# Kernel tuning notes

Measured on AMD Instinct MI355X. Metric: run time of the kernel, lower is better.

## Reference

```python
import jax, jax.numpy as jnp
import numpy as np

B, T, E, H = 4, 2048, 1024, 16
HS = E // H  # head_size = 64
FFN_HID = 100  # hard-coded in FeedForward
EPS = 1e-5


def layernorm(x, g, b):
    mu = jnp.mean(x, axis=-1, keepdims=True)
    var = jnp.mean(jnp.square(x - mu), axis=-1, keepdims=True)
    return (x - mu) * jax.lax.rsqrt(var + EPS) * g + b


def setup_inputs() -> dict:
    key = jax.random.key(0)
    ks = jax.random.split(key, 10)
    s = E ** -0.5
    return {
        "x": jax.random.normal(ks[0], (B, T, E), jnp.float32),
        "wq": jax.random.normal(ks[1], (E, E), jnp.float32) * s,
        "wk": jax.random.normal(ks[2], (E, E), jnp.float32) * s,
        "wv": jax.random.normal(ks[3], (E, E), jnp.float32) * s,
        "w_proj": jax.random.normal(ks[4], (E, E), jnp.float32) * s,
        "b_proj": jnp.zeros((E,), jnp.float32),
        "w1": jax.random.normal(ks[5], (E, FFN_HID), jnp.float32) * s,
        "b1": jnp.zeros((FFN_HID,), jnp.float32),
        "w2": jax.random.normal(ks[6], (FFN_HID, E), jnp.float32) * (FFN_HID ** -0.5),
        "b2": jnp.zeros((E,), jnp.float32),
        "ln1_g": jnp.ones((E,), jnp.float32),
        "ln1_b": jnp.zeros((E,), jnp.float32),
        "ln2_g": jnp.ones((E,), jnp.float32),
        "ln2_b": jnp.zeros((E,), jnp.float32),
    }


def reference(x, wq, wk, wv, w_proj, b_proj, w1, b1, w2, b2, ln1_g, ln1_b, ln2_g, ln2_b):
    # --- self-attention with pre-LN residual ---
    h = layernorm(x, ln1_g, ln1_b)  # [B,T,E]
    def split_heads(y):  # [B,T,E] -> [B,H,T,HS]
        return y.reshape(B, T, H, HS).transpose(0, 2, 1, 3)
    q = split_heads(h @ wq)
    k = split_heads(h @ wk)
    v = split_heads(h @ wv)
    # NOTE: original scales by C**-0.5 with C = n_embd (not head_size)
    wei = jnp.einsum("bhtd,bhsd->bhts", q, k) * (E ** -0.5)  # [B,H,T,T]
    causal = jnp.tril(jnp.ones((T, T), bool))
    wei = jnp.where(causal, wei, -jnp.inf)
    wei = jax.nn.softmax(wei, axis=-1)
    att = jnp.einsum("bhts,bhsd->bhtd", wei, v)  # [B,H,T,HS]
    att = att.transpose(0, 2, 1, 3).reshape(B, T, E)  # concat heads
    x = x + att @ w_proj + b_proj
    # --- feedforward with pre-LN residual ---
    h2 = layernorm(x, ln2_g, ln2_b)
    ff = jax.nn.relu(h2 @ w1 + b1) @ w2 + b2
    return x + ff
```

## Files before the change

### kernel.cpp

```cpp
#include <hip/hip_runtime.h>

typedef unsigned short u16;
typedef unsigned int u32;
typedef __bf16 bf16x8 __attribute__((ext_vector_type(8)));
typedef float f32x4 __attribute__((ext_vector_type(4)));

#define BDIM 4
#define TDIM 2048
#define EDIM 1024
#define HDIM 16
#define HS 64
#define MROWS (BDIM * TDIM)
#define FFNP 128

__device__ __forceinline__ u16 f2bf(float f) {
    __bf16 h = (__bf16)f;
    return __builtin_bit_cast(u16, h);
}

__device__ __forceinline__ float bf2f(u16 u) {
    return (float)__builtin_bit_cast(__bf16, u);
}

__device__ __forceinline__ void glds16(const void* g, void* l) {
    __builtin_amdgcn_global_load_lds(
        (__attribute__((address_space(1))) const void*)g,
        (__attribute__((address_space(3))) void*)l, 16, 0, 0);
}

__global__ __launch_bounds__(256) void transpose_all(
    const float* __restrict__ wq, const float* __restrict__ wk,
    const float* __restrict__ wv, const float* __restrict__ wproj,
    const float* __restrict__ w1, const float* __restrict__ w2,
    u16* __restrict__ wqkvt, u16* __restrict__ wpt,
    u16* __restrict__ w1t, u16* __restrict__ w2t)
{
    __shared__ u16 sm[64][72];
    const float* src; u16* dst;
    int K, N, Kpad, Npad;
    switch (blockIdx.z) {
        case 0: src = wq;    dst = wqkvt;                 K = N = Kpad = Npad = 1024; break;
        case 1: src = wk;    dst = wqkvt + 1024 * 1024;   K = N = Kpad = Npad = 1024; break;
        case 2: src = wv;    dst = wqkvt + 2 * 1024 * 1024; K = N = Kpad = Npad = 1024; break;
        case 3: src = wproj; dst = wpt;                   K = N = Kpad = Npad = 1024; break;
        case 4: src = w1;    dst = w1t; K = 1024; N = 100; Kpad = 1024; Npad = 128; break;
        default: src = w2;   dst = w2t; K = 100; N = 1024; Kpad = 128; Npad = 1024; break;
    }
    int k0 = blockIdx.x * 64, n0 = blockIdx.y * 64;
    if (k0 >= Kpad || n0 >= Npad) return;
    int tid = threadIdx.x;
#pragma unroll
    for (int i = 0; i < 16; i++) {
        int idx = i * 256 + tid;
        int kl = idx >> 6, nl = idx & 63;
        int k = k0 + kl, n = n0 + nl;
        float v = (k < K && n < N) ? src[(size_t)k * N + n] : 0.f;
        sm[kl][nl] = f2bf(v);
    }
    __syncthreads();
#pragma unroll
    for (int i = 0; i < 16; i++) {
        int idx = i * 256 + tid;
        int nl = idx >> 6, kl = idx & 63;
        int n = n0 + nl, k = k0 + kl;
        if (n < Npad && k < Kpad) dst[(size_t)n * Kpad + k] = sm[kl][nl];
    }
}

__global__ __launch_bounds__(256) void ln_rows(
    const float* __restrict__ X, const float* __restrict__ G,
    const float* __restrict__ Bv, u16* __restrict__ H)
{
    int w = threadIdx.x >> 6, l = threadIdx.x & 63;
    int row = blockIdx.x * 4 + w;
    const float* xr = X + (size_t)row * EDIM;
    float4 v[4];
    float s = 0.f, s2 = 0.f;
#pragma unroll
    for (int i = 0; i < 4; i++) {
        v[i] = *(const float4*)&xr[l * 4 + i * 256];
        s += v[i].x + v[i].y + v[i].z + v[i].w;
        s2 += v[i].x * v[i].x + v[i].y * v[i].y + v[i].z * v[i].z + v[i].w * v[i].w;
    }
#pragma unroll
    for (int off = 1; off < 64; off <<= 1) {
        s += __shfl_xor(s, off, 64);
        s2 += __shfl_xor(s2, off, 64);
    }
    float mean = s * (1.f / EDIM);
    float var = s2 * (1.f / EDIM) - mean * mean;
    float rstd = rsqrtf(var + 1e-5f);
#pragma unroll
    for (int i = 0; i < 4; i++) {
        int c = l * 4 + i * 256;
        float4 gg = *(const float4*)&G[c];
        float4 bb = *(const float4*)&Bv[c];
        u16 o0 = f2bf((v[i].x - mean) * rstd * gg.x + bb.x);
        u16 o1 = f2bf((v[i].y - mean) * rstd * gg.y + bb.y);
        u16 o2 = f2bf((v[i].z - mean) * rstd * gg.z + bb.z);
        u16 o3 = f2bf((v[i].w - mean) * rstd * gg.w + bb.w);
        uint2 pk;
        pk.x = (u32)o0 | ((u32)o1 << 16);
        pk.y = (u32)o2 | ((u32)o3 << 16);
        *(uint2*)&H[(size_t)row * EDIM + c] = pk;
    }
}

__global__ __launch_bounds__(256) void ln_rows_b(
    const u16* __restrict__ X, const float* __restrict__ G,
    const float* __restrict__ Bv, u16* __restrict__ H)
{
    int w = threadIdx.x >> 6, l = threadIdx.x & 63;
    int row = blockIdx.x * 4 + w;
    const u16* xr = X + (size_t)row * EDIM;
    float v[16];
    float s = 0.f, s2 = 0.f;
#pragma unroll
    for (int i = 0; i < 2; i++) {
        bf16x8 u = *(const bf16x8*)&xr[l * 8 + i * 512];
#pragma unroll
        for (int e = 0; e < 8; e++) {
            float f = (float)u[e];
            v[i * 8 + e] = f;
            s += f; s2 += f * f;
        }
    }
#pragma unroll
    for (int off = 1; off < 64; off <<= 1) {
        s += __shfl_xor(s, off, 64);
        s2 += __shfl_xor(s2, off, 64);
    }
    float mean = s * (1.f / EDIM);
    float var = s2 * (1.f / EDIM) - mean * mean;
    float rstd = rsqrtf(var + 1e-5f);
#pragma unroll
    for (int i = 0; i < 2; i++) {
        int c = l * 8 + i * 512;
        float4 g0 = *(const float4*)&G[c];
        float4 g1 = *(const float4*)&G[c + 4];
        float4 b0 = *(const float4*)&Bv[c];
        float4 b1 = *(const float4*)&Bv[c + 4];
        float gg[8] = {g0.x, g0.y, g0.z, g0.w, g1.x, g1.y, g1.z, g1.w};
        float bb[8] = {b0.x, b0.y, b0.z, b0.w, b1.x, b1.y, b1.z, b1.w};
        uint4 pk;
        u32 o[8];
#pragma unroll
        for (int e = 0; e < 8; e++)
            o[e] = (u32)f2bf((v[i * 8 + e] - mean) * rstd * gg[e] + bb[e]);
        pk.x = o[0] | (o[1] << 16);
        pk.y = o[2] | (o[3] << 16);
        pk.z = o[4] | (o[5] << 16);
        pk.w = o[6] | (o[7] << 16);
        *(uint4*)&H[(size_t)row * EDIM + c] = pk;
    }
}

#define LDA4(d, mfb)                                                          \
    _Pragma("unroll") for (int mi = 0; mi < 4; mi++)                          \
    _Pragma("unroll") for (int ks = 0; ks < 2; ks++)                          \
        a[mi][ks] = *(const bf16x8*)&L[d][0][wm][((mfb + mi) * 16 + lr) * 64  \
                        + (((lg + 4 * ks) ^ (lr & 7)) << 3)];
#define LDB2(d, nfb)                                                          \
    _Pragma("unroll") for (int ni = 0; ni < 2; ni++)                          \
    _Pragma("unroll") for (int ks = 0; ks < 2; ks++)                          \
        b[ni][ks] = *(const bf16x8*)&L[d][1][wh][((wn & 1) * 64               \
                        + (nfb + ni) * 16 + lr) * 64                          \
                        + (((lg + 4 * ks) ^ (lr & 7)) << 3)];
#define MFMAQ(mfb, nfb)                                                       \
    _Pragma("unroll") for (int mi = 0; mi < 4; mi++)                          \
    _Pragma("unroll") for (int ni = 0; ni < 2; ni++)                          \
    _Pragma("unroll") for (int ks = 0; ks < 2; ks++)                          \
        acc[mfb + mi][nfb + ni] = __builtin_amdgcn_mfma_f32_16x16x32_bf16(    \
            a[mi][ks], b[ni][ks], acc[mfb + mi][nfb + ni], 0, 0, 0);
#define PH_SYNC1()                                                            \
    __builtin_amdgcn_s_barrier();                                             \
    asm volatile("s_waitcnt lgkmcnt(0)" ::: "memory");                        \
    __builtin_amdgcn_sched_barrier(0);                                        \
    __builtin_amdgcn_s_setprio(1);
#define PH_SYNC2()                                                            \
    __builtin_amdgcn_s_setprio(0);                                            \
    __builtin_amdgcn_s_barrier();
#define PH_SYNC2V(cond)                                                       \
    __builtin_amdgcn_s_setprio(0);                                            \
    if (cond) { asm volatile("s_waitcnt vmcnt(2)" ::: "memory"); }            \
    else      { asm volatile("s_waitcnt vmcnt(0)" ::: "memory"); }            \
    __builtin_amdgcn_s_barrier();

__global__ __launch_bounds__(512, 2) void gemm256_qk(
    const u16* __restrict__ A, const u16* __restrict__ Bt,
    u16* __restrict__ Cb)
{
    __shared__ u16 L[2][2][2][128 * 64];
    int id = blockIdx.x;
    int sw = (id & 7) * 32 + (id >> 3);
    int bx = sw % 32, by = sw / 32;
    const int m0 = bx * 256, n0 = by * 256;

    const int tid = threadIdx.x;
    const int w = tid >> 6, l = tid & 63;
    const int wm = w >> 2, wn = w & 3, wh = wn >> 1;
    const int lg = l >> 4, lr = l & 15;

    const int srow = w * 16 + (l >> 3);
    const int sch8 = ((l & 7) ^ (l >> 3)) * 8;

    auto stA = [&](int d, int h, int t) {
        const u16* src = A + (size_t)(m0 + h * 128 + srow) * 1024 + t * 64 + sch8;
        u16* dst = &L[d][0][h][w * 1024];
        glds16(src, dst);
        glds16(src + (size_t)8 * 1024, dst + 512);
    };
    auto stB = [&](int d, int h, int t) {
        const u16* src = Bt + (size_t)(n0 + h * 128 + srow) * 1024 + t * 64 + sch8;
        u16* dst = &L[d][1][h][w * 1024];
        glds16(src, dst);
        glds16(src + (size_t)8 * 1024, dst + 512);
    };

    f32x4 acc[8][4];
#pragma unroll
    for (int i = 0; i < 8; i++)
#pragma unroll
        for (int j = 0; j < 4; j++) acc[i][j] = f32x4{0.f, 0.f, 0.f, 0.f};
    bf16x8 a[4][2], b[2][2];

    const int NI = 1024 >> 7;

    stA(0, 0, 0); stA(0, 1, 0); stB(0, 0, 0); stB(0, 1, 0);
    stB(1, 0, 1);
    asm volatile("s_waitcnt vmcnt(2)" ::: "memory");
    __builtin_amdgcn_s_barrier();

#pragma unroll 1
    for (int j = 0; j < NI; j++) {
        const int t = 2 * j;
        const bool more = (j + 1 < NI);
        LDA4(0, 0); LDB2(0, 0);
        stA(1, 0, t + 1);
        PH_SYNC1(); MFMAQ(0, 0); PH_SYNC2();
        LDA4(0, 4);
        stA(1, 1, t + 1);
        PH_SYNC1(); MFMAQ(4, 0); PH_SYNC2();
        LDB2(0, 2);
        stB(1, 1, t + 1);
        PH_SYNC1(); MFMAQ(4, 2); PH_SYNC2();
        LDA4(0, 0);
        if (more) stB(0, 1, t + 2);
        PH_SYNC1(); MFMAQ(0, 2); PH_SYNC2V(more);
        LDA4(1, 0); LDB2(1, 0);
        if (more) stA(0, 0, t + 2);
        PH_SYNC1(); MFMAQ(0, 0); PH_SYNC2();
        LDA4(1, 4);
        if (more) stA(0, 1, t + 2);
        PH_SYNC1(); MFMAQ(4, 0); PH_SYNC2();
        LDB2(1, 2);
        if (more) stB(0, 0, t + 2);
        PH_SYNC1(); MFMAQ(4, 2); PH_SYNC2();
        LDA4(1, 0);
        if (more) stB(1, 0, t + 3);
        PH_SYNC1(); MFMAQ(0, 2); PH_SYNC2V(more);
    }

#pragma unroll
    for (int mf = 0; mf < 8; mf++) {
#pragma unroll
        for (int nf = 0; nf < 4; nf++) {
#pragma unroll
            for (int e = 0; e < 4; e++) {
                int row = m0 + wm * 128 + mf * 16 + lg * 4 + e;
                int col = n0 + wn * 64 + nf * 16 + lr;
                Cb[(size_t)row * 2048 + col] = f2bf(acc[mf][nf][e]);
            }
        }
    }
}

template <int MODE>
__global__ __launch_bounds__(256, 2) void gemm_bt(
    const u16* __restrict__ A, const u16* __restrict__ Bt,
    float* __restrict__ Cf,
    const void* __restrict__ resid, const float* __restrict__ bias,
    int M, int N, int K, int lda, int ldb, int mb)
{
    __shared__ u16 As[2][128 * 32];
    __shared__ u16 Bs[2][128 * 32];
    int bx, by;
    if constexpr (MODE == 4) {
        bx = blockIdx.x; by = blockIdx.y;
        int kz = blockIdx.z;
        A += kz * 256;
        Bt += kz * 256;
        Cf += (size_t)kz * M * N;
    } else {
        int nwg = gridDim.x, id = blockIdx.x;
        int sw = (id & 7) * (nwg >> 3) + (id >> 3);
        bx = sw % mb; by = sw / mb;
    }
    const int tid = threadIdx.x;
    const int w = tid >> 6, l = tid & 63;
    const int wr = w >> 1, wc = w & 1;
    const int lg = l >> 4, lr = l & 15;
    const int m0 = bx * 128, n0 = by * 128;

    f32x4 zero = {0.f, 0.f, 0.f, 0.f};
    f32x4 acc[4][4];
#pragma unroll
    for (int i = 0; i < 4; i++)
#pragma unroll
        for (int j = 0; j < 4; j++) acc[i][j] = zero;

    const u16* Ag = A + (size_t)(m0 + w * 16 + (l >> 2)) * lda + (l & 3) * 8;
    const u16* Bg = Bt + (size_t)(n0 + w * 16 + (l >> 2)) * ldb + (l & 3) * 8;

    auto stage = [&](int b, int k0) {
        glds16(Ag + k0, &As[b][w * 512]);
        glds16(Ag + k0 + (size_t)64 * lda, &As[b][w * 512 + 2048]);
        glds16(Bg + k0, &Bs[b][w * 512]);
        glds16(Bg + k0 + (size_t)64 * ldb, &Bs[b][w * 512 + 2048]);
    };
    auto compute = [&](int b) {
        bf16x8 af[4], bfr[4];
#pragma unroll
        for (int t = 0; t < 4; t++)
            af[t] = *(const bf16x8*)&As[b][(wr * 64 + t * 16 + lr) * 32 + lg * 8];
#pragma unroll
        for (int t = 0; t < 4; t++)
            bfr[t] = *(const bf16x8*)&Bs[b][(wc * 64 + t * 16 + lr) * 32 + lg * 8];
#pragma unroll
        for (int i = 0; i < 4; i++)
#pragma unroll
            for (int j = 0; j < 4; j++)
                acc[i][j] = __builtin_amdgcn_mfma_f32_16x16x32_bf16(
                    af[i], bfr[j], acc[i][j], 0, 0, 0);
    };

    stage(0, 0);
    __syncthreads();
    int cur = 0;
    for (int k0 = 32; k0 < K; k0 += 32) {
        stage(cur ^ 1, k0);
        compute(cur);
        __syncthreads();
        cur ^= 1;
    }
    compute(cur);

#pragma unroll
    for (int i = 0; i < 4; i++) {
#pragma unroll
        for (int j = 0; j < 4; j++) {
#pragma unroll
            for (int e = 0; e < 4; e++) {
                int row = m0 + wr * 64 + i * 16 + lg * 4 + e;
                int col = n0 + wc * 64 + j * 16 + lr;
                float v = acc[i][j][e];
                if constexpr (MODE == 2) {
                    size_t idx = (size_t)row * N + col;
                    ((u16*)Cf)[idx] =
                        f2bf(((const float*)resid)[idx] + v + bias[col]);
                } else if constexpr (MODE == 3) {
                    size_t idx = (size_t)row * N + col;
                    Cf[idx] = bf2f(((const u16*)resid)[idx]) + v + bias[col];
                } else if constexpr (MODE == 4) {
                    Cf[(size_t)row * N + col] = v;
                } else {
                    u16* vtp = (u16*)Cf;
                    int bq = col >> 11, tt = col & 2047;
                    vtp[((size_t)bq * 1024 + row) * 2048 + tt] = f2bf(v);
                }
            }
        }
    }
}

__global__ __launch_bounds__(256) void relu_reduce4(
    const float* __restrict__ fp, const float* __restrict__ b1,
    u16* __restrict__ tb)
{
    const size_t CH = (size_t)MROWS * FFNP;
    size_t base = ((size_t)blockIdx.x * 256 + threadIdx.x) * 4;
    float4 s0 = *(const float4*)&fp[base];
    float4 s1 = *(const float4*)&fp[base + CH];
    float4 s2 = *(const float4*)&fp[base + 2 * CH];
    float4 s3 = *(const float4*)&fp[base + 3 * CH];
    int col = (int)(base & (FFNP - 1));
    float sv[4] = {s0.x + s1.x + s2.x + s3.x, s0.y + s1.y + s2.y + s3.y,
                   s0.z + s1.z + s2.z + s3.z, s0.w + s1.w + s2.w + s3.w};
    u16 o[4];
#pragma unroll
    for (int j = 0; j < 4; j++) {
        int c = col + j;
        float b = (c < 100) ? b1[c] : 0.f;
        o[j] = f2bf(fmaxf(sv[j] + b, 0.f));
    }
    uint2 pk;
    pk.x = (u32)o[0] | ((u32)o[1] << 16);
    pk.y = (u32)o[2] | ((u32)o[3] << 16);
    *(uint2*)&tb[base] = pk;
}

__global__ __launch_bounds__(256, 4) void attn_fwd(
    const u16* __restrict__ qk, const u16* __restrict__ Vt,
    u16* __restrict__ Og)
{
    int xcd = blockIdx.x & 7;
    int j = blockIdx.x >> 3;
    int bh = xcd * 8 + (j & 7);
    int qp = j >> 3;
    int bb = bh >> 4, hh = bh & 15;

    int tid = threadIdx.x;
    int w = tid >> 6, l = tid & 63;
    int lg = l >> 4, lr = l & 15;

    const u16* Qb = qk + ((size_t)bb * TDIM) * 2048 + hh * HS;
    const u16* Kb = Qb + 1024;
    const u16* Vb = Vt + (size_t)bh * HS * TDIM;

    __shared__ u16 Ks[2][64 * 64];
    __shared__ u16 Vs[2][64 * 64];
    __shared__ __align__(16) u16 Ps[4][16 * 64];

    int srow = w * 16 + (l >> 3);
    int schunk = (l & 7) ^ ((l >> 3) & 7);
    u16* Pw = Ps[w];
    int sbase = (l & 48) + lg * 4;

    const float QSCL = 0.045084227f;

#pragma unroll 1
    for (int qi = 0; qi < 2; qi++) {
        int qb = (qi == 0 ? qp : 31 - qp) * 64;
        int q_abs = qb + w * 16 + lr;
        int wlo = qb + w * 16;
        int nt = qb / 64 + 1;

        bf16x8 qf[2];
        qf[0] = *(const bf16x8*)&Qb[(size_t)q_abs * 2048 + lg * 8];
        qf[1] = *(const bf16x8*)&Qb[(size_t)q_abs * 2048 + 32 + lg * 8];
#pragma unroll
        for (int i = 0; i < 8; i++) {
            qf[0][i] = (__bf16)((float)qf[0][i] * QSCL);
            qf[1][i] = (__bf16)((float)qf[1][i] * QSCL);
        }

        f32x4 zero = {0.f, 0.f, 0.f, 0.f};
        f32x4 oacc[4];
#pragma unroll
        for (int dt = 0; dt < 4; dt++) oacc[dt] = zero;
        float lpart = 0.f;

        auto stage = [&](int b, int kv0) {
            glds16(Kb + (size_t)(kv0 + srow) * 2048 + schunk * 8, &Ks[b][w * 1024]);
            glds16(Kb + (size_t)(kv0 + srow + 8) * 2048 + schunk * 8,
                   &Ks[b][w * 1024 + 512]);
            glds16(Vb + (size_t)srow * TDIM + kv0 + schunk * 8, &Vs[b][w * 1024]);
            glds16(Vb + (size_t)(srow + 8) * TDIM + kv0 + schunk * 8,
                   &Vs[b][w * 1024 + 512]);
        };

        stage(0, 0);
        if (nt > 1) stage(1, 64);
#pragma unroll 1
        for (int t = 0; t < nt; t++) {
            int kv0 = t * 64;
            int buf = t & 1;
            if (t + 1 < nt) { asm volatile("s_waitcnt vmcnt(4)" ::: "memory"); }
            else            { asm volatile("s_waitcnt vmcnt(0)" ::: "memory"); }
            __builtin_amdgcn_sched_barrier(0);
            __builtin_amdgcn_s_barrier();
            const u16* Kc = Ks[buf];
            const u16* Vc = Vs[buf];
            f32x4 sc[4];
#pragma unroll
            for (int ct = 0; ct < 4; ct++) sc[ct] = zero;
            __builtin_amdgcn_s_setprio(1);
#pragma unroll
            for (int ct = 0; ct < 4; ct++) {
#pragma unroll
                for (int dc = 0; dc < 2; dc++) {
                    bf16x8 kf = *(const bf16x8*)&Kc[(ct * 16 + lr) * 64 +
                                                    (((lg + 4 * dc) ^ (lr & 7)) << 3)];
                    sc[ct] = __builtin_amdgcn_mfma_f32_16x16x32_bf16(
                        kf, qf[dc], sc[ct], 0, 0, 0);
                }
            }
            __builtin_amdgcn_s_setprio(0);
            bf16x8 vfr[2][4];
#pragma unroll
            for (int m = 0; m < 2; m++)
#pragma unroll
                for (int dt = 0; dt < 4; dt++)
                    vfr[m][dt] = *(const bf16x8*)&Vc[(dt * 16 + lr) * 64 +
                                                     (((lg + 4 * m) ^ (lr & 7)) << 3)];
            float p[16];
            if (kv0 + 63 > wlo) {
#pragma unroll
                for (int ct = 0; ct < 4; ct++) {
#pragma unroll
                    for (int e = 0; e < 4; e++) {
                        float v = sc[ct][e];
                        if (kv0 + ct * 16 + lg * 4 + e > q_abs) v = -1e30f;
                        p[ct * 4 + e] = v;
                    }
                }
            } else {
#pragma unroll
                for (int ct = 0; ct < 4; ct++) {
#pragma unroll
                    for (int e = 0; e < 4; e++) p[ct * 4 + e] = sc[ct][e];
                }
            }
            float psum = 0.f;
#pragma unroll
            for (int i = 0; i < 16; i++) {
                p[i] = __builtin_amdgcn_exp2f(p[i]);
                psum += p[i];
            }
            lpart += psum;
#pragma unroll
            for (int ct = 0; ct < 4; ct++) {
                uint2 pr;
                pr.x = (u32)f2bf(p[ct * 4 + 0]) | ((u32)f2bf(p[ct * 4 + 1]) << 16);
                pr.y = (u32)f2bf(p[ct * 4 + 2]) | ((u32)f2bf(p[ct * 4 + 3]) << 16);
                int kvb = ct * 16 + lg * 4;
                int idx = lr * 64 + ((((kvb >> 3) ^ (lr & 7)) << 3) | (kvb & 7));
                *(uint2*)&Pw[idx] = pr;
            }
            asm volatile("s_waitcnt lgkmcnt(0)" ::: "memory");
            __builtin_amdgcn_sched_barrier(0);
            __builtin_amdgcn_s_setprio(1);
#pragma unroll
            for (int m = 0; m < 2; m++) {
                bf16x8 pa = *(const bf16x8*)&Pw[lr * 64 + (((lg + 4 * m) ^ (lr & 7)) << 3)];
#pragma unroll
                for (int dt = 0; dt < 4; dt++) {
                    oacc[dt] = __builtin_amdgcn_mfma_f32_16x16x32_bf16(
                        pa, vfr[m][dt], oacc[dt], 0, 0, 0);
                }
            }
            __builtin_amdgcn_s_setprio(0);
            __builtin_amdgcn_s_barrier();
            if (t + 2 < nt) stage(buf, kv0 + 128);
        }
        float lsum = lpart;
        lsum += __shfl_xor(lsum, 16, 64);
        lsum += __shfl_xor(lsum, 32, 64);
        float lT[4];
#pragma unroll
        for (int e = 0; e < 4; e++) lT[e] = __shfl(lsum, sbase + e, 64);
#pragma unroll
        for (int dt = 0; dt < 4; dt++) {
#pragma unroll
            for (int e = 0; e < 4; e++) {
                int row = qb + w * 16 + lg * 4 + e;
                Og[((size_t)bb * TDIM + row) * EDIM + hh * HS + dt * 16 + lr] =
                    f2bf(oacc[dt][e] / lT[e]);
            }
        }
    }
}

extern "C" void kernel_launch(void* const* d_in, const int* in_sizes, int n_in,
                              void* d_out, int out_size, void* d_ws, size_t ws_size,
                              hipStream_t stream)
{
    const float* x     = (const float*)d_in[0];
    const float* wq    = (const float*)d_in[1];
    const float* wk    = (const float*)d_in[2];
    const float* wv    = (const float*)d_in[3];
    const float* wproj = (const float*)d_in[4];
    const float* bproj = (const float*)d_in[5];
    const float* w1    = (const float*)d_in[6];
    const float* b1    = (const float*)d_in[7];
    const float* w2    = (const float*)d_in[8];
    const float* b2    = (const float*)d_in[9];
    const float* ln1g  = (const float*)d_in[10];
    const float* ln1b  = (const float*)d_in[11];
    const float* ln2g  = (const float*)d_in[12];
    const float* ln2b  = (const float*)d_in[13];
    float* out = (float*)d_out;

    char* ws = (char*)d_ws;
    size_t off = 0;
    auto alloc = [&](size_t bytes) -> void* {
        void* p = (void*)(ws + off);
        off += (bytes + 255) & ~(size_t)255;
        return p;
    };
    u16* hbuf = (u16*)alloc((size_t)MROWS * EDIM * 2);
    u16* qk   = (u16*)alloc((size_t)MROWS * 2048 * 2);
    u16* attb = (u16*)alloc((size_t)MROWS * EDIM * 2);
    u16* vt   = (u16*)alloc((size_t)MROWS * EDIM * 2);
    u16* x2b  = (u16*)alloc((size_t)MROWS * EDIM * 2);
    u16* wqkvt = (u16*)alloc((size_t)3072 * EDIM * 2);
    u16* wpt  = (u16*)alloc((size_t)EDIM * EDIM * 2);
    u16* w1t  = (u16*)alloc((size_t)FFNP * EDIM * 2);
    u16* w2t  = (u16*)alloc((size_t)EDIM * FFNP * 2);
    float* fp = (float*)qk;
    u16* tb   = vt;

    transpose_all<<<dim3(16, 16, 6), 256, 0, stream>>>(
        wq, wk, wv, wproj, w1, w2, wqkvt, wpt, w1t, w2t);

    ln_rows<<<MROWS / 4, 256, 0, stream>>>(x, ln1g, ln1b, hbuf);
    gemm256_qk<<<dim3(256), 512, 0, stream>>>(hbuf, wqkvt, qk);
    gemm_bt<5><<<dim3(512), 256, 0, stream>>>(wqkvt + (size_t)2048 * 1024, hbuf,
                                              (float*)vt, nullptr, nullptr,
                                              1024, 8192, 1024, 1024, 1024, 8);
    attn_fwd<<<dim3(1024), 256, 0, stream>>>(qk, vt, attb);
    gemm_bt<2><<<dim3(512), 256, 0, stream>>>(attb, wpt, (float*)x2b, x, bproj,
                                              MROWS, EDIM, EDIM, EDIM, EDIM, 64);
    ln_rows_b<<<MROWS / 4, 256, 0, stream>>>(x2b, ln2g, ln2b, hbuf);
    gemm_bt<4><<<dim3(64, 1, 4), 256, 0, stream>>>(hbuf, w1t, fp, nullptr, nullptr,
                                                   MROWS, FFNP, 256, EDIM, EDIM, 64);
    relu_reduce4<<<dim3(MROWS * FFNP / 1024), 256, 0, stream>>>(fp, b1, tb);
    gemm_bt<3><<<dim3(512), 256, 0, stream>>>(tb, w2t, out, x2b, b2,
                                              MROWS, EDIM, FFNP, FFNP, FFNP, 64);
}
```

Before: 210.8 us.

## Load V fragments directly from global in attention; store split-K FFN partials as bf16

```diff
diff --git a/kernel.cpp b/kernel.cpp
--- a/kernel.cpp
+++ b/kernel.cpp
@@ -290,7 +290,7 @@
         int kz = blockIdx.z;
         A += kz * 256;
         Bt += kz * 256;
-        Cf += (size_t)kz * M * N;
+        Cf = (float*)((u16*)Cf + (size_t)kz * M * N);
     } else {
         int nwg = gridDim.x, id = blockIdx.x;
         int sw = (id & 7) * (nwg >> 3) + (id >> 3);
@@ -362,7 +362,7 @@
                     size_t idx = (size_t)row * N + col;
                     Cf[idx] = bf2f(((const u16*)resid)[idx]) + v + bias[col];
                 } else if constexpr (MODE == 4) {
-                    Cf[(size_t)row * N + col] = v;
+                    ((u16*)Cf)[(size_t)row * N + col] = f2bf(v);
                 } else {
                     u16* vtp = (u16*)Cf;
                     int bq = col >> 11, tt = col & 2047;
@@ -374,29 +374,30 @@
 }
 
 __global__ __launch_bounds__(256) void relu_reduce4(
-    const float* __restrict__ fp, const float* __restrict__ b1,
+    const u16* __restrict__ fp, const float* __restrict__ b1,
     u16* __restrict__ tb)
 {
     const size_t CH = (size_t)MROWS * FFNP;
-    size_t base = ((size_t)blockIdx.x * 256 + threadIdx.x) * 4;
-    float4 s0 = *(const float4*)&fp[base];
-    float4 s1 = *(const float4*)&fp[base + CH];
-    float4 s2 = *(const float4*)&fp[base + 2 * CH];
-    float4 s3 = *(const float4*)&fp[base + 3 * CH];
+    size_t base = ((size_t)blockIdx.x * 256 + threadIdx.x) * 8;
+    bf16x8 s0 = *(const bf16x8*)&fp[base];
+    bf16x8 s1 = *(const bf16x8*)&fp[base + CH];
+    bf16x8 s2 = *(const bf16x8*)&fp[base + 2 * CH];
+    bf16x8 s3 = *(const bf16x8*)&fp[base + 3 * CH];
     int col = (int)(base & (FFNP - 1));
-    float sv[4] = {s0.x + s1.x + s2.x + s3.x, s0.y + s1.y + s2.y + s3.y,
-                   s0.z + s1.z + s2.z + s3.z, s0.w + s1.w + s2.w + s3.w};
-    u16 o[4];
-#pragma unroll
-    for (int j = 0; j < 4; j++) {
+    u32 o[8];
+#pragma unroll
+    for (int j = 0; j < 8; j++) {
+        float sv = (float)s0[j] + (float)s1[j] + (float)s2[j] + (float)s3[j];
         int c = col + j;
         float b = (c < 100) ? b1[c] : 0.f;
-        o[j] = f2bf(fmaxf(sv[j] + b, 0.f));
-    }
-    uint2 pk;
-    pk.x = (u32)o[0] | ((u32)o[1] << 16);
-    pk.y = (u32)o[2] | ((u32)o[3] << 16);
-    *(uint2*)&tb[base] = pk;
+        o[j] = (u32)f2bf(fmaxf(sv + b, 0.f));
+    }
+    uint4 pk;
+    pk.x = o[0] | (o[1] << 16);
+    pk.y = o[2] | (o[3] << 16);
+    pk.z = o[4] | (o[5] << 16);
+    pk.w = o[6] | (o[7] << 16);
+    *(uint4*)&tb[base] = pk;
 }
 
 __global__ __launch_bounds__(256, 4) void attn_fwd(
@@ -418,7 +419,6 @@
     const u16* Vb = Vt + (size_t)bh * HS * TDIM;
 
     __shared__ u16 Ks[2][64 * 64];
-    __shared__ u16 Vs[2][64 * 64];
     __shared__ __align__(16) u16 Ps[4][16 * 64];
 
     int srow = w * 16 + (l >> 3);
@@ -450,27 +450,29 @@
         for (int dt = 0; dt < 4; dt++) oacc[dt] = zero;
         float lpart = 0.f;
 
-        auto stage = [&](int b, int kv0) {
+        auto stageK = [&](int b, int kv0) {
             glds16(Kb + (size_t)(kv0 + srow) * 2048 + schunk * 8, &Ks[b][w * 1024]);
             glds16(Kb + (size_t)(kv0 + srow + 8) * 2048 + schunk * 8,
                    &Ks[b][w * 1024 + 512]);
-            glds16(Vb + (size_t)srow * TDIM + kv0 + schunk * 8, &Vs[b][w * 1024]);
-            glds16(Vb + (size_t)(srow + 8) * TDIM + kv0 + schunk * 8,
-                   &Vs[b][w * 1024 + 512]);
         };
 
-        stage(0, 0);
-        if (nt > 1) stage(1, 64);
+        stageK(0, 0);
+        if (nt > 1) stageK(1, 64);
 #pragma unroll 1
         for (int t = 0; t < nt; t++) {
             int kv0 = t * 64;
             int buf = t & 1;
-            if (t + 1 < nt) { asm volatile("s_waitcnt vmcnt(4)" ::: "memory"); }
-            else            { asm volatile("s_waitcnt vmcnt(0)" ::: "memory"); }
+            asm volatile("s_waitcnt vmcnt(2)" ::: "memory");
             __builtin_amdgcn_sched_barrier(0);
             __builtin_amdgcn_s_barrier();
             const u16* Kc = Ks[buf];
-            const u16* Vc = Vs[buf];
+            bf16x8 vfr[2][4];
+#pragma unroll
+            for (int m = 0; m < 2; m++)
+#pragma unroll
+                for (int dt = 0; dt < 4; dt++)
+                    vfr[m][dt] = *(const bf16x8*)&Vb[(size_t)(dt * 16 + lr) * TDIM +
+                                                     kv0 + (lg + 4 * m) * 8];
             f32x4 sc[4];
 #pragma unroll
             for (int ct = 0; ct < 4; ct++) sc[ct] = zero;
@@ -486,13 +488,6 @@
                 }
             }
             __builtin_amdgcn_s_setprio(0);
-            bf16x8 vfr[2][4];
-#pragma unroll
-            for (int m = 0; m < 2; m++)
-#pragma unroll
-                for (int dt = 0; dt < 4; dt++)
-                    vfr[m][dt] = *(const bf16x8*)&Vc[(dt * 16 + lr) * 64 +
-                                                     (((lg + 4 * m) ^ (lr & 7)) << 3)];
             float p[16];
             if (kv0 + 63 > wlo) {
 #pragma unroll
@@ -541,7 +536,7 @@
             }
             __builtin_amdgcn_s_setprio(0);
             __builtin_amdgcn_s_barrier();
-            if (t + 2 < nt) stage(buf, kv0 + 128);
+            if (t + 2 < nt) stageK(buf, kv0 + 128);
         }
         float lsum = lpart;
         lsum += __shfl_xor(lsum, 16, 64);
@@ -597,8 +592,8 @@
     u16* wpt  = (u16*)alloc((size_t)EDIM * EDIM * 2);
     u16* w1t  = (u16*)alloc((size_t)FFNP * EDIM * 2);
     u16* w2t  = (u16*)alloc((size_t)EDIM * FFNP * 2);
-    float* fp = (float*)qk;
-    u16* tb   = vt;
+    u16* fpb = (u16*)qk;
+    u16* tb  = vt;
 
     transpose_all<<<dim3(16, 16, 6), 256, 0, stream>>>(
         wq, wk, wv, wproj, w1, w2, wqkvt, wpt, w1t, w2t);
@@ -612,9 +607,10 @@
     gemm_bt<2><<<dim3(512), 256, 0, stream>>>(attb, wpt, (float*)x2b, x, bproj,
                                               MROWS, EDIM, EDIM, EDIM, EDIM, 64);
     ln_rows_b<<<MROWS / 4, 256, 0, stream>>>(x2b, ln2g, ln2b, hbuf);
-    gemm_bt<4><<<dim3(64, 1, 4), 256, 0, stream>>>(hbuf, w1t, fp, nullptr, nullptr,
-                                                   MROWS, FFNP, 256, EDIM, EDIM, 64);
-    relu_reduce4<<<dim3(MROWS * FFNP / 1024), 256, 0, stream>>>(fp, b1, tb);
+    gemm_bt<4><<<dim3(64, 1, 4), 256, 0, stream>>>(hbuf, w1t, (float*)fpb, nullptr,
+                                                   nullptr, MROWS, FFNP, 256,
+                                                   EDIM, EDIM, 64);
+    relu_reduce4<<<dim3(MROWS * FFNP / 2048), 256, 0, stream>>>(fpb, b1, tb);
     gemm_bt<3><<<dim3(512), 256, 0, stream>>>(tb, w2t, out, x2b, b2,
                                               MROWS, EDIM, FFNP, FFNP, FFNP, 64);
 }
```

Measured after the change: 288.7 us. 1.37x slower.
